# Kernel tuning notes

Measured on AMD Instinct MI355X. Metric: run time of the kernel, lower is better.

## Reference

```python
import jax, jax.numpy as jnp
import numpy as np

K = 5  # topk hyperedges per node (hardcoded in module)
EPS_DEG = 1e-6
EPS_PD = 1e-6  # torch F.pairwise_distance eps added to the difference


def _safe_normalize(t):
    n = jnp.linalg.norm(t, axis=1, keepdims=True)
    n = jnp.where(n > 0, n, jnp.ones_like(n))
    return t / n


def _hyper_proj(x, W, b, centers, alpha):
    # mlp: Linear + Tanh
    x_proj = jnp.tanh(x @ W.T + b)                      # [N, d]
    # cosine similarity to hyperedge centers
    sim = jnp.clip(_safe_normalize(x_proj) @ _safe_normalize(centers).T, -1.0, 1.0)  # [N, E]
    N, E = sim.shape
    vals, idx = jax.lax.top_k(sim, K)                   # [N, K]
    rows = jnp.repeat(jnp.arange(N), K)
    # sparse incidence H as a thin dense [N, E] (E is small: 64)
    H = jnp.zeros((N, E), dtype=x_proj.dtype).at[rows, idx.reshape(-1)].set(vals.reshape(-1))
    # degree normalization
    D_v = H.sum(axis=1)                                 # [N]
    D_e = H.sum(axis=0)                                 # [E]
    dv_inv_sqrt = 1.0 / (jnp.sqrt(D_v) + EPS_DEG)
    de_inv = 1.0 / (D_e + EPS_DEG)
    step1 = x_proj * dv_inv_sqrt[:, None]               # [N, d]
    step2 = H.T @ step1                                 # [E, d]
    step3 = step2 * de_inv[:, None]
    step4 = H @ step3                                   # [N, d]
    step5 = step4 * dv_inv_sqrt[:, None]
    x_hyper = (1.0 - alpha) * x_proj + alpha * step5
    return x_proj + x_hyper


def _pairwise_distance(x1, x2):
    # torch F.pairwise_distance: ||x1 - x2 + eps||_2 per row
    return jnp.linalg.norm(x1 - x2 + EPS_PD, axis=1)


def setup_inputs() -> dict:
    key = jax.random.key(0)
    ks = jax.random.split(key, 6)
    N, F_in, D, E = 100000, 256, 128, 64
    return {
        "anchor": jax.random.normal(ks[0], (N, F_in), dtype=jnp.float32),
        "positive": jax.random.normal(ks[1], (N, F_in), dtype=jnp.float32),
        "negative": jax.random.normal(ks[2], (N, F_in), dtype=jnp.float32),
        "W": jax.random.normal(ks[3], (D, F_in), dtype=jnp.float32) * 0.05,
        "b": jax.random.normal(ks[4], (D,), dtype=jnp.float32) * 0.05,
        "centers": jax.random.normal(ks[5], (E, D), dtype=jnp.float32),
        "alpha": jnp.float32(0.5),
    }


def reference(anchor, positive, negative, W, b, centers, alpha):
    a = _hyper_proj(anchor, W, b, centers, alpha)
    p = _hyper_proj(positive, W, b, centers, alpha)
    n = _hyper_proj(negative, W, b, centers, alpha)
    dis = _pairwise_distance(a, n) - _pairwise_distance(a, p)
    return (a, p, n, dis)
```

## Files before the change

kernel.cpp:

```cpp
#include <hip/hip_runtime.h>
#include <math.h>

#define K_TOP 5
#define E_NUM 64
#define D_DIM 128
#define F_DIM 256
#define TM 64
#define SC_WAVES 2

typedef __attribute__((ext_vector_type(8))) short bf16x8;
typedef __attribute__((ext_vector_type(4))) float f32x4;

__device__ __forceinline__ short f2bf(float f) {
  union { float f; unsigned u; } v; v.f = f;
  unsigned r = v.u + 0x7fffu + ((v.u >> 16) & 1u);
  return (short)(r >> 16);
}

__device__ __forceinline__ float fast_tanh(float x) {
  float e = __expf(2.0f * x);
  return 1.0f - 2.0f / (e + 1.0f);
}

__global__ void k_wconv(const float* __restrict__ W, short* __restrict__ Wbf, int n) {
  int i = blockIdx.x * 256 + threadIdx.x;
  if (i < n) Wbf[i] = f2bf(W[i]);
}

__global__ void k_centers(const float* __restrict__ C, short* __restrict__ cnbf) {
  __shared__ float ws2[2];
  int e = blockIdx.x, t = threadIdx.x;
  float v = C[e * D_DIM + t];
  float s = v * v;
  s += __shfl_down(s, 32); s += __shfl_down(s, 16); s += __shfl_down(s, 8);
  s += __shfl_down(s, 4);  s += __shfl_down(s, 2);  s += __shfl_down(s, 1);
  if ((t & 63) == 0) ws2[t >> 6] = s;
  __syncthreads();
  float n = sqrtf(ws2[0] + ws2[1]);
  n = (n > 0.f) ? n : 1.f;
  cnbf[e * D_DIM + t] = f2bf(v / n);
}

__global__ void k_zero(float* __restrict__ p, int n) {
  int i = blockIdx.x * 256 + threadIdx.x;
  if (i < n) p[i] = 0.f;
}

__launch_bounds__(256)
__global__ void k_phaseA(const float* __restrict__ x0, const float* __restrict__ x1,
                         const float* __restrict__ x2,
                         const short* __restrict__ Wbf, const float* __restrict__ bvec,
                         const short* __restrict__ cnbf,
                         float* __restrict__ out,
                         float* __restrict__ vals_ws, int* __restrict__ idx_ws,
                         float* __restrict__ dvis_ws, int N)
{
  __shared__ __align__(16) char smem[33792 + 17408 + 256];
  short (*A)[264]  = (short(*)[264])smem;
  float (*xp)[132] = (float(*)[132])smem;
  float (*sim)[68] = (float(*)[68])(smem + 33792);
  float* rinv      = (float*)(smem + 33792 + 17408);

  const int t = threadIdx.x;
  const int s = blockIdx.y;
  const float* x = (s == 0) ? x0 : ((s == 1) ? x1 : x2);
  const int r0 = blockIdx.x * TM;
  const int m = min(TM, N - r0);
  float* out_s = out + (size_t)s * N * D_DIM;

  #pragma unroll
  for (int i = 0; i < 16; ++i) {
    int f4 = t + i * 256;
    int row = f4 >> 6, c4 = f4 & 63;
    float4 v = make_float4(0.f, 0.f, 0.f, 0.f);
    if (row < m) v = *(const float4*)(x + (size_t)(r0 + row) * F_DIM + (c4 << 2));
    short4 sv; sv.x = f2bf(v.x); sv.y = f2bf(v.y); sv.z = f2bf(v.z); sv.w = f2bf(v.w);
    *(short4*)&A[row][c4 << 2] = sv;
  }
  __syncthreads();

  const int w = t >> 6, l = t & 63;
  const int lrow = l & 15;
  const int lk8  = (l >> 4) << 3;
  const int colbase = w << 5;

  f32x4 acc[4][2];
  #pragma unroll
  for (int a_ = 0; a_ < 4; ++a_)
    #pragma unroll
    for (int b_ = 0; b_ < 2; ++b_)
      #pragma unroll
      for (int q = 0; q < 4; ++q) acc[a_][b_][q] = 0.f;

  #pragma unroll
  for (int kk = 0; kk < 8; ++kk) {
    const int k = (kk << 5) + lk8;
    bf16x8 af[4], bfr[2];
    #pragma unroll
    for (int rt = 0; rt < 4; ++rt)
      af[rt] = *(const bf16x8*)&A[(rt << 4) + lrow][k];
    #pragma unroll
    for (int ct = 0; ct < 2; ++ct)
      bfr[ct] = *(const bf16x8*)(Wbf + (size_t)(colbase + (ct << 4) + lrow) * F_DIM + k);
    #pragma unroll
    for (int rt = 0; rt < 4; ++rt)
      #pragma unroll
      for (int ct = 0; ct < 2; ++ct)
        acc[rt][ct] = __builtin_amdgcn_mfma_f32_16x16x32_bf16(af[rt], bfr[ct], acc[rt][ct], 0, 0, 0);
  }
  __syncthreads();

  #pragma unroll
  for (int ct = 0; ct < 2; ++ct) {
    const int col = colbase + (ct << 4) + lrow;
    const float bb = bvec[col];
    #pragma unroll
    for (int rt = 0; rt < 4; ++rt)
      #pragma unroll
      for (int q = 0; q < 4; ++q) {
        int row = (rt << 4) + ((l >> 4) << 2) + q;
        xp[row][col] = fast_tanh(acc[rt][ct][q] + bb);
      }
  }
  __syncthreads();

  #pragma unroll
  for (int i = 0; i < 8; ++i) {
    int f4 = t + i * 256;
    int row = f4 >> 5, c4 = f4 & 31;
    if (row < m) {
      float4 v;
      v.x = xp[row][(c4 << 2)];     v.y = xp[row][(c4 << 2) + 1];
      v.z = xp[row][(c4 << 2) + 2]; v.w = xp[row][(c4 << 2) + 3];
      *(float4*)(out_s + (size_t)(r0 + row) * D_DIM + (c4 << 2)) = v;
    }
  }
  {
    int row = t >> 2, q = t & 3;
    float ss = 0.f;
    #pragma unroll
    for (int j = 0; j < 32; ++j) { float v = xp[row][(q << 5) + j]; ss += v * v; }
    ss += __shfl_xor(ss, 1);
    ss += __shfl_xor(ss, 2);
    if (q == 0) { float nn = sqrtf(ss); rinv[row] = 1.f / ((nn > 0.f) ? nn : 1.f); }
  }
  __syncthreads();

  const int ebase = w << 4;
  f32x4 acc2[4];
  #pragma unroll
  for (int rt = 0; rt < 4; ++rt)
    #pragma unroll
    for (int q = 0; q < 4; ++q) acc2[rt][q] = 0.f;

  #pragma unroll
  for (int kk = 0; kk < 4; ++kk) {
    const int k = (kk << 5) + lk8;
    bf16x8 bc = *(const bf16x8*)(cnbf + (size_t)(ebase + lrow) * D_DIM + k);
    #pragma unroll
    for (int rt = 0; rt < 4; ++rt) {
      const float* src = &xp[(rt << 4) + lrow][k];
      float4 a0 = *(const float4*)(src);
      float4 a1 = *(const float4*)(src + 4);
      bf16x8 af;
      af[0] = f2bf(a0.x); af[1] = f2bf(a0.y); af[2] = f2bf(a0.z); af[3] = f2bf(a0.w);
      af[4] = f2bf(a1.x); af[5] = f2bf(a1.y); af[6] = f2bf(a1.z); af[7] = f2bf(a1.w);
      acc2[rt] = __builtin_amdgcn_mfma_f32_16x16x32_bf16(af, bc, acc2[rt], 0, 0, 0);
    }
  }
  #pragma unroll
  for (int rt = 0; rt < 4; ++rt)
    #pragma unroll
    for (int q = 0; q < 4; ++q)
      sim[(rt << 4) + ((l >> 4) << 2) + q][ebase + lrow] = acc2[rt][q];
  __syncthreads();

  if (t < m) {
    const int row = t;
    const float rv = rinv[row];
    float v0 = -2.f, v1 = -2.f, v2 = -2.f, v3 = -2.f, v4 = -2.f;
    int i0 = 0, i1 = 0, i2 = 0, i3 = 0, i4 = 0;
    for (int e = 0; e < E_NUM; ++e) {
      float v = sim[row][e] * rv;
      v = fminf(fmaxf(v, -1.f), 1.f);
      if (v > v4) {
        if (v > v0)      { v4=v3;i4=i3; v3=v2;i3=i2; v2=v1;i2=i1; v1=v0;i1=i0; v0=v; i0=e; }
        else if (v > v1) { v4=v3;i4=i3; v3=v2;i3=i2; v2=v1;i2=i1; v1=v; i1=e; }
        else if (v > v2) { v4=v3;i4=i3; v3=v2;i3=i2; v2=v; i2=e; }
        else if (v > v3) { v4=v3;i4=i3; v3=v; i3=e; }
        else             { v4=v; i4=e; }
      }
    }
    float Dv = v0 + v1 + v2 + v3 + v4;
    float dvq = 1.f / (sqrtf(Dv) + 1e-6f);
    size_t gr = (size_t)s * N + (r0 + row);
    dvis_ws[gr] = dvq;
    float* vp = vals_ws + gr * 5;
    int*   ip = idx_ws  + gr * 5;
    vp[0]=v0; vp[1]=v1; vp[2]=v2; vp[3]=v3; vp[4]=v4;
    ip[0]=i0; ip[1]=i1; ip[2]=i2; ip[3]=i3; ip[4]=i4;
  }
}

__launch_bounds__(128)
__global__ void k_scatter(const float* __restrict__ out,
                          const float* __restrict__ vals_ws, const int* __restrict__ idx_ws,
                          const float* __restrict__ dvis_ws,
                          float* __restrict__ De_g, float* __restrict__ step2_g,
                          int N, int P)
{
  __shared__ float s2[SC_WAVES][E_NUM][64];
  __shared__ float de[SC_WAVES][E_NUM];
  const int t = threadIdx.x;
  const int wid = t >> 6, l = t & 63;
  const int s = blockIdx.y;
  const int half = blockIdx.z;
  const int d0 = half << 6;

  for (int i = t; i < SC_WAVES * E_NUM * 64; i += 128) ((float*)s2)[i] = 0.f;
  for (int i = t; i < SC_WAVES * E_NUM; i += 128) ((float*)de)[i] = 0.f;
  __syncthreads();

  const int chunk = (N + P - 1) / P;
  const int rbeg = blockIdx.x * chunk;
  const int rend = min(N, rbeg + chunk);
  const float* xps = out + (size_t)s * N * D_DIM + d0;
  float (*m2)[64] = s2[wid];
  float* mde = de[wid];

#define LOADROW(rr, X, DV, V0, V1, V2, V3, V4, E0, E1, E2, E3, E4) { \
    size_t gr_ = (size_t)s * N + (rr); \
    X = xps[(size_t)(rr) * D_DIM + l]; \
    DV = dvis_ws[gr_]; \
    const float* vp_ = vals_ws + gr_ * 5; \
    const int*   ip_ = idx_ws  + gr_ * 5; \
    V0 = vp_[0]; V1 = vp_[1]; V2 = vp_[2]; V3 = vp_[3]; V4 = vp_[4]; \
    E0 = ip_[0]; E1 = ip_[1]; E2 = ip_[2]; E3 = ip_[3]; E4 = ip_[4]; }

  int r = rbeg + wid;
  float xv = 0.f, dv = 0.f, va0 = 0.f, va1 = 0.f, va2 = 0.f, va3 = 0.f, va4 = 0.f;
  int ea0 = 0, ea1 = 0, ea2 = 0, ea3 = 0, ea4 = 0;
  if (r < rend) LOADROW(r, xv, dv, va0, va1, va2, va3, va4, ea0, ea1, ea2, ea3, ea4);
  while (r < rend) {
    const int rn = r + SC_WAVES;
    float xn = 0.f, dn = 0.f, w0 = 0.f, w1 = 0.f, w2 = 0.f, w3 = 0.f, w4 = 0.f;
    int f0 = 0, f1 = 0, f2 = 0, f3 = 0, f4 = 0;
    if (rn < rend) LOADROW(rn, xn, dn, w0, w1, w2, w3, w4, f0, f1, f2, f3, f4);
    const float st1 = xv * dv;
    m2[ea0][l] += va0 * st1;
    m2[ea1][l] += va1 * st1;
    m2[ea2][l] += va2 * st1;
    m2[ea3][l] += va3 * st1;
    m2[ea4][l] += va4 * st1;
    if (half == 0 && l == 0) {
      mde[ea0] += va0; mde[ea1] += va1; mde[ea2] += va2; mde[ea3] += va3; mde[ea4] += va4;
    }
    xv = xn; dv = dn;
    va0 = w0; va1 = w1; va2 = w2; va3 = w3; va4 = w4;
    ea0 = f0; ea1 = f1; ea2 = f2; ea3 = f3; ea4 = f4;
    r = rn;
  }
#undef LOADROW

  __syncthreads();
  for (int i = t; i < E_NUM * 64; i += 128) {
    int e = i >> 6, dd = i & 63;
    float v = s2[0][e][dd] + s2[1][e][dd];
    atomicAdd(&step2_g[((size_t)s * E_NUM + e) * D_DIM + d0 + dd], v);
  }
  if (half == 0) {
    for (int i = t; i < E_NUM; i += 128)
      atomicAdd(&De_g[s * E_NUM + i], de[0][i] + de[1][i]);
  }
}

__global__ void k_step3(const float* __restrict__ step2_g, const float* __restrict__ De_g,
                        float* __restrict__ step3_g) {
  int i = blockIdx.x * 256 + threadIdx.x;
  if (i < 3 * E_NUM * D_DIM) {
    int s = i / (E_NUM * D_DIM);
    int e = (i / D_DIM) % E_NUM;
    step3_g[i] = step2_g[i] / (De_g[s * E_NUM + e] + 1e-6f);
  }
}

__launch_bounds__(256)
__global__ void k_combine(float* __restrict__ out, const float* __restrict__ vals_ws,
                          const int* __restrict__ idx_ws, const float* __restrict__ dvis_ws,
                          const float* __restrict__ step3_g, const float* __restrict__ alpha_p,
                          int N)
{
  const float alpha = *alpha_p;
  const float ca = 2.0f - alpha;
  const int t = threadIdx.x;
  const int lane = t & 31;
  const int rg = t >> 5;
  const int d0 = lane << 2;
  const int ngroups = (N + 7) / 8;
  for (int g = blockIdx.x; g < ngroups; g += (int)gridDim.x) {
    int r = g * 8 + rg;
    if (r >= N) continue;
    float fa0=0,fa1=0,fa2=0,fa3=0;
    float sp = 0.f, sn = 0.f;
    #pragma unroll
    for (int s = 0; s < 3; ++s) {
      size_t gr = (size_t)s * N + r;
      float dv = dvis_ws[gr];
      const float* vp = vals_ws + gr * 5;
      const int*   ip = idx_ws  + gr * 5;
      float* op = out + gr * D_DIM + d0;
      float4 xv = *(const float4*)op;
      float h0=0,h1=0,h2=0,h3=0;
      const float* s3 = step3_g + (size_t)s * E_NUM * D_DIM;
      #pragma unroll
      for (int k = 0; k < K_TOP; ++k) {
        float val = vp[k]; int e = ip[k];
        float4 sr = *(const float4*)(s3 + (size_t)e * D_DIM + d0);
        h0 += val * sr.x; h1 += val * sr.y; h2 += val * sr.z; h3 += val * sr.w;
      }
      float adv = alpha * dv;
      float f0 = ca * xv.x + adv * h0;
      float f1 = ca * xv.y + adv * h1;
      float f2 = ca * xv.z + adv * h2;
      float f3 = ca * xv.w + adv * h3;
      *(float4*)op = make_float4(f0, f1, f2, f3);
      if (s == 0) { fa0=f0; fa1=f1; fa2=f2; fa3=f3; }
      else if (s == 1) {
        float d_;
        d_ = fa0-f0+1e-6f; sp += d_*d_;  d_ = fa1-f1+1e-6f; sp += d_*d_;
        d_ = fa2-f2+1e-6f; sp += d_*d_;  d_ = fa3-f3+1e-6f; sp += d_*d_;
      } else {
        float d_;
        d_ = fa0-f0+1e-6f; sn += d_*d_;  d_ = fa1-f1+1e-6f; sn += d_*d_;
        d_ = fa2-f2+1e-6f; sn += d_*d_;  d_ = fa3-f3+1e-6f; sn += d_*d_;
      }
    }
    sp += __shfl_xor(sp, 1); sp += __shfl_xor(sp, 2); sp += __shfl_xor(sp, 4);
    sp += __shfl_xor(sp, 8); sp += __shfl_xor(sp, 16);
    sn += __shfl_xor(sn, 1); sn += __shfl_xor(sn, 2); sn += __shfl_xor(sn, 4);
    sn += __shfl_xor(sn, 8); sn += __shfl_xor(sn, 16);
    if (lane == 0) out[(size_t)3 * N * D_DIM + r] = sqrtf(sn) - sqrtf(sp);
  }
}

extern "C" void kernel_launch(void* const* d_in, const int* in_sizes, int n_in,
                              void* d_out, int out_size, void* d_ws, size_t ws_size,
                              hipStream_t stream) {
  const float* xa      = (const float*)d_in[0];
  const float* xpos    = (const float*)d_in[1];
  const float* xn      = (const float*)d_in[2];
  const float* W       = (const float*)d_in[3];
  const float* bvec    = (const float*)d_in[4];
  const float* centers = (const float*)d_in[5];
  const float* alpha   = (const float*)d_in[6];
  float* out = (float*)d_out;
  const int N = in_sizes[0] / F_DIM;

  char* ws = (char*)d_ws;
  short* Wbf   = (short*)(ws);
  short* cnbf  = (short*)(ws + 65536);
  float* De_g  = (float*)(ws + 81920);
  float* step2 = (float*)(ws + 82688);
  float* step3 = (float*)(ws + 180992);
  size_t o = 279296;
  float* vals = (float*)(ws + o); o += (size_t)3 * N * 5 * 4;
  int*   idxs = (int*)(ws + o);   o += (size_t)3 * N * 5 * 4;
  float* dvis = (float*)(ws + o);

  k_wconv<<<(D_DIM * F_DIM + 255) / 256, 256, 0, stream>>>(W, Wbf, D_DIM * F_DIM);
  k_centers<<<E_NUM, D_DIM, 0, stream>>>(centers, cnbf);
  k_zero<<<(24768 + 255) / 256, 256, 0, stream>>>(De_g, 24768);

  dim3 gA((N + TM - 1) / TM, 3);
  k_phaseA<<<gA, 256, 0, stream>>>(xa, xpos, xn, Wbf, bvec, cnbf, out, vals, idxs, dvis, N);

  const int P = 170;
  k_scatter<<<dim3(P, 3, 2), 128, 0, stream>>>(out, vals, idxs, dvis, De_g, step2, N, P);
  k_step3<<<(3 * E_NUM * D_DIM + 255) / 256, 256, 0, stream>>>(step2, De_g, step3);
  k_combine<<<2048, 256, 0, stream>>>(out, vals, idxs, dvis, step3, alpha, N);
}
```

Baseline: 812.6 us.

## Restructure phaseA similarity and top-k into register-resident wave-parallel path

```diff
diff --git a/kernel.cpp b/kernel.cpp
--- a/kernel.cpp
+++ b/kernel.cpp
@@ -15,6 +15,11 @@
   union { float f; unsigned u; } v; v.f = f;
   unsigned r = v.u + 0x7fffu + ((v.u >> 16) & 1u);
   return (short)(r >> 16);
+}
+
+__device__ __forceinline__ float bf2f(short h) {
+  union { unsigned u; float f; } v; v.u = ((unsigned)(unsigned short)h) << 16;
+  return v.f;
 }
 
 __device__ __forceinline__ float fast_tanh(float x) {
@@ -46,7 +51,7 @@
   if (i < n) p[i] = 0.f;
 }
 
-__launch_bounds__(256)
+__launch_bounds__(256, 4)
 __global__ void k_phaseA(const float* __restrict__ x0, const float* __restrict__ x1,
                          const float* __restrict__ x2,
                          const short* __restrict__ Wbf, const float* __restrict__ bvec,
@@ -55,11 +60,9 @@
                          float* __restrict__ vals_ws, int* __restrict__ idx_ws,
                          float* __restrict__ dvis_ws, int N)
 {
-  __shared__ __align__(16) char smem[33792 + 17408 + 256];
-  short (*A)[264]  = (short(*)[264])smem;
-  float (*xp)[132] = (float(*)[132])smem;
-  float (*sim)[68] = (float(*)[68])(smem + 33792);
-  float* rinv      = (float*)(smem + 33792 + 17408);
+  __shared__ __align__(16) char smem[33792];
+  short (*A)[264]   = (short(*)[264])smem;
+  short (*xpb)[136] = (short(*)[136])smem;
 
   const int t = threadIdx.x;
   const int s = blockIdx.y;
@@ -74,14 +77,17 @@
     int row = f4 >> 6, c4 = f4 & 63;
     float4 v = make_float4(0.f, 0.f, 0.f, 0.f);
     if (row < m) v = *(const float4*)(x + (size_t)(r0 + row) * F_DIM + (c4 << 2));
-    short4 sv; sv.x = f2bf(v.x); sv.y = f2bf(v.y); sv.z = f2bf(v.z); sv.w = f2bf(v.w);
-    *(short4*)&A[row][c4 << 2] = sv;
+    unsigned p01, p23;
+    asm("v_cvt_pk_bf16_f32 %0, %1, %2" : "=v"(p01) : "v"(v.x), "v"(v.y));
+    asm("v_cvt_pk_bf16_f32 %0, %1, %2" : "=v"(p23) : "v"(v.z), "v"(v.w));
+    *(uint2*)&A[row][c4 << 2] = make_uint2(p01, p23);
   }
   __syncthreads();
 
   const int w = t >> 6, l = t & 63;
   const int lrow = l & 15;
   const int lk8  = (l >> 4) << 3;
+  const int g4   = (l >> 4) << 2;
   const int colbase = w << 5;
 
   f32x4 acc[4][2];
@@ -118,87 +124,89 @@
     for (int rt = 0; rt < 4; ++rt)
       #pragma unroll
       for (int q = 0; q < 4; ++q) {
-        int row = (rt << 4) + ((l >> 4) << 2) + q;
-        xp[row][col] = fast_tanh(acc[rt][ct][q] + bb);
+        int row = (rt << 4) + g4 + q;
+        float v = fast_tanh(acc[rt][ct][q] + bb);
+        if (row < m) out_s[(size_t)(r0 + row) * D_DIM + col] = v;
+        xpb[row][col] = f2bf(v);
       }
   }
   __syncthreads();
 
-  #pragma unroll
-  for (int i = 0; i < 8; ++i) {
-    int f4 = t + i * 256;
-    int row = f4 >> 5, c4 = f4 & 31;
+  const int rowbase = w << 4;
+  f32x4 acc2[4];
+  #pragma unroll
+  for (int et = 0; et < 4; ++et)
+    #pragma unroll
+    for (int q = 0; q < 4; ++q) acc2[et][q] = 0.f;
+
+  float ss = 0.f;
+  #pragma unroll
+  for (int kt = 0; kt < 4; ++kt) {
+    const int k = (kt << 5) + lk8;
+    bf16x8 bx = *(const bf16x8*)&xpb[rowbase + lrow][k];
+    #pragma unroll
+    for (int j = 0; j < 8; ++j) { float f = bf2f(bx[j]); ss += f * f; }
+    #pragma unroll
+    for (int et = 0; et < 4; ++et) {
+      bf16x8 bc = *(const bf16x8*)(cnbf + (size_t)((et << 4) + lrow) * D_DIM + k);
+      acc2[et] = __builtin_amdgcn_mfma_f32_16x16x32_bf16(bc, bx, acc2[et], 0, 0, 0);
+    }
+  }
+  ss += __shfl_xor(ss, 16);
+  ss += __shfl_xor(ss, 32);
+  float nn = sqrtf(ss);
+  const float rv = 1.f / ((nn > 0.f) ? nn : 1.f);
+
+  float bv0 = -2.f, bv1 = -2.f, bv2 = -2.f, bv3 = -2.f, bv4 = -2.f;
+  int   bi0 = 64,   bi1 = 64,   bi2 = 64,   bi3 = 64,   bi4 = 64;
+  #pragma unroll
+  for (int et = 0; et < 4; ++et)
+    #pragma unroll
+    for (int q = 0; q < 4; ++q) {
+      float v = acc2[et][q] * rv;
+      v = fminf(fmaxf(v, -1.f), 1.f);
+      int e = (et << 4) + g4 + q;
+      bool c0 = v > bv0, c1 = v > bv1, c2 = v > bv2, c3 = v > bv3, c4 = v > bv4;
+      bv4 = c4 ? (c3 ? bv3 : v) : bv4;  bi4 = c4 ? (c3 ? bi3 : e) : bi4;
+      bv3 = c3 ? (c2 ? bv2 : v) : bv3;  bi3 = c3 ? (c2 ? bi2 : e) : bi3;
+      bv2 = c2 ? (c1 ? bv1 : v) : bv2;  bi2 = c2 ? (c1 ? bi1 : e) : bi2;
+      bv1 = c1 ? (c0 ? bv0 : v) : bv1;  bi1 = c1 ? (c0 ? bi0 : e) : bi1;
+      bv0 = c0 ? v : bv0;               bi0 = c0 ? e : bi0;
+    }
+
+  #pragma unroll
+  for (int mm = 16; mm <= 32; mm <<= 1) {
+    float ov0 = __shfl_xor(bv0, mm), ov1 = __shfl_xor(bv1, mm), ov2 = __shfl_xor(bv2, mm),
+          ov3 = __shfl_xor(bv3, mm), ov4 = __shfl_xor(bv4, mm);
+    int   oi0 = __shfl_xor(bi0, mm), oi1 = __shfl_xor(bi1, mm), oi2 = __shfl_xor(bi2, mm),
+          oi3 = __shfl_xor(bi3, mm), oi4 = __shfl_xor(bi4, mm);
+    #define INS2(vv, ii) { \
+      bool c0 = (vv > bv0) || (vv == bv0 && ii < bi0); \
+      bool c1 = (vv > bv1) || (vv == bv1 && ii < bi1); \
+      bool c2 = (vv > bv2) || (vv == bv2 && ii < bi2); \
+      bool c3 = (vv > bv3) || (vv == bv3 && ii < bi3); \
+      bool c4 = (vv > bv4) || (vv == bv4 && ii < bi4); \
+      bv4 = c4 ? (c3 ? bv3 : vv) : bv4;  bi4 = c4 ? (c3 ? bi3 : ii) : bi4; \
+      bv3 = c3 ? (c2 ? bv2 : vv) : bv3;  bi3 = c3 ? (c2 ? bi2 : ii) : bi3; \
+      bv2 = c2 ? (c1 ? bv1 : vv) : bv2;  bi2 = c2 ? (c1 ? bi1 : ii) : bi2; \
+      bv1 = c1 ? (c0 ? bv0 : vv) : bv1;  bi1 = c1 ? (c0 ? bi0 : ii) : bi1; \
+      bv0 = c0 ? vv : bv0;               bi0 = c0 ? ii : bi0; }
+    INS2(ov0, oi0); INS2(ov1, oi1); INS2(ov2, oi2); INS2(ov3, oi3); INS2(ov4, oi4);
+    #undef INS2
+  }
+
+  if (l < 16) {
+    int row = rowbase + l;
     if (row < m) {
-      float4 v;
-      v.x = xp[row][(c4 << 2)];     v.y = xp[row][(c4 << 2) + 1];
-      v.z = xp[row][(c4 << 2) + 2]; v.w = xp[row][(c4 << 2) + 3];
-      *(float4*)(out_s + (size_t)(r0 + row) * D_DIM + (c4 << 2)) = v;
-    }
-  }
-  {
-    int row = t >> 2, q = t & 3;
-    float ss = 0.f;
-    #pragma unroll
-    for (int j = 0; j < 32; ++j) { float v = xp[row][(q << 5) + j]; ss += v * v; }
-    ss += __shfl_xor(ss, 1);
-    ss += __shfl_xor(ss, 2);
-    if (q == 0) { float nn = sqrtf(ss); rinv[row] = 1.f / ((nn > 0.f) ? nn : 1.f); }
-  }
-  __syncthreads();
-
-  const int ebase = w << 4;
-  f32x4 acc2[4];
-  #pragma unroll
-  for (int rt = 0; rt < 4; ++rt)
-    #pragma unroll
-    for (int q = 0; q < 4; ++q) acc2[rt][q] = 0.f;
-
-  #pragma unroll
-  for (int kk = 0; kk < 4; ++kk) {
-    const int k = (kk << 5) + lk8;
-    bf16x8 bc = *(const bf16x8*)(cnbf + (size_t)(ebase + lrow) * D_DIM + k);
-    #pragma unroll
-    for (int rt = 0; rt < 4; ++rt) {
-      const float* src = &xp[(rt << 4) + lrow][k];
-      float4 a0 = *(const float4*)(src);
-      float4 a1 = *(const float4*)(src + 4);
-      bf16x8 af;
-      af[0] = f2bf(a0.x); af[1] = f2bf(a0.y); af[2] = f2bf(a0.z); af[3] = f2bf(a0.w);
-      af[4] = f2bf(a1.x); af[5] = f2bf(a1.y); af[6] = f2bf(a1.z); af[7] = f2bf(a1.w);
-      acc2[rt] = __builtin_amdgcn_mfma_f32_16x16x32_bf16(af, bc, acc2[rt], 0, 0, 0);
-    }
-  }
-  #pragma unroll
-  for (int rt = 0; rt < 4; ++rt)
-    #pragma unroll
-    for (int q = 0; q < 4; ++q)
-      sim[(rt << 4) + ((l >> 4) << 2) + q][ebase + lrow] = acc2[rt][q];
-  __syncthreads();
-
-  if (t < m) {
-    const int row = t;
-    const float rv = rinv[row];
-    float v0 = -2.f, v1 = -2.f, v2 = -2.f, v3 = -2.f, v4 = -2.f;
-    int i0 = 0, i1 = 0, i2 = 0, i3 = 0, i4 = 0;
-    for (int e = 0; e < E_NUM; ++e) {
-      float v = sim[row][e] * rv;
-      v = fminf(fmaxf(v, -1.f), 1.f);
-      if (v > v4) {
-        if (v > v0)      { v4=v3;i4=i3; v3=v2;i3=i2; v2=v1;i2=i1; v1=v0;i1=i0; v0=v; i0=e; }
-        else if (v > v1) { v4=v3;i4=i3; v3=v2;i3=i2; v2=v1;i2=i1; v1=v; i1=e; }
-        else if (v > v2) { v4=v3;i4=i3; v3=v2;i3=i2; v2=v; i2=e; }
-        else if (v > v3) { v4=v3;i4=i3; v3=v; i3=e; }
-        else             { v4=v; i4=e; }
-      }
-    }
-    float Dv = v0 + v1 + v2 + v3 + v4;
-    float dvq = 1.f / (sqrtf(Dv) + 1e-6f);
-    size_t gr = (size_t)s * N + (r0 + row);
-    dvis_ws[gr] = dvq;
-    float* vp = vals_ws + gr * 5;
-    int*   ip = idx_ws  + gr * 5;
-    vp[0]=v0; vp[1]=v1; vp[2]=v2; vp[3]=v3; vp[4]=v4;
-    ip[0]=i0; ip[1]=i1; ip[2]=i2; ip[3]=i3; ip[4]=i4;
+      float Dv = bv0 + bv1 + bv2 + bv3 + bv4;
+      float dvq = 1.f / (sqrtf(Dv) + 1e-6f);
+      size_t gr = (size_t)s * N + (r0 + row);
+      dvis_ws[gr] = dvq;
+      float* vp = vals_ws + gr * 5;
+      int*   ip = idx_ws  + gr * 5;
+      vp[0] = bv0; vp[1] = bv1; vp[2] = bv2; vp[3] = bv3; vp[4] = bv4;
+      ip[0] = bi0; ip[1] = bi1; ip[2] = bi2; ip[3] = bi3; ip[4] = bi4;
+    }
   }
 }
 
```

Result: faster. 746.0 us (-8.2%).
